# Performance work log

Hardware: AMD Instinct MI355X
Metric: run time of the kernel (lower is better)

Reference implementation:

```python
import jax, jax.numpy as jnp
import numpy as np

B, T, C = 4, 2048, 1024
N_HEAD = 16
HEAD_SIZE = C // N_HEAD


def setup_inputs() -> dict:
    key = jax.random.key(0)
    ks = jax.random.split(key, 9)
    std = 0.02
    return {
        "x": jax.random.normal(ks[0], (B, T, C), dtype=jnp.float32),
        "Wk": jax.random.normal(ks[1], (C, C), dtype=jnp.float32) * std,
        "bk": jnp.zeros((C,), dtype=jnp.float32),
        "Wq": jax.random.normal(ks[2], (C, C), dtype=jnp.float32) * std,
        "bq": jnp.zeros((C,), dtype=jnp.float32),
        "Wv": jax.random.normal(ks[3], (C, C), dtype=jnp.float32) * std,
        "bv": jnp.zeros((C,), dtype=jnp.float32),
        "Wo": jax.random.normal(ks[4], (C, C), dtype=jnp.float32) * std,
        "bo": jnp.zeros((C,), dtype=jnp.float32),
    }


def reference(x, Wk, bk, Wq, bq, Wv, bv, Wo, bo):
    # QKV projections -> (B, T, H, D)
    k = (x @ Wk + bk).reshape(B, T, N_HEAD, HEAD_SIZE)
    q = (x @ Wq + bq).reshape(B, T, N_HEAD, HEAD_SIZE)
    v = (x @ Wv + bv).reshape(B, T, N_HEAD, HEAD_SIZE)
    # Scaled causal attention scores: (B, H, T, T)
    scale = 1.0 / jnp.sqrt(jnp.asarray(HEAD_SIZE, dtype=x.dtype))
    scores = jnp.einsum("bqhd,bkhd->bhqk", q, k) * scale
    causal = jnp.tril(jnp.ones((T, T), dtype=bool))
    scores = jnp.where(causal, scores, jnp.asarray(-1e10, dtype=x.dtype))
    probs = jax.nn.softmax(scores, axis=-1)
    # Weighted values -> (B, T, H, D) -> (B, T, C)
    y = jnp.einsum("bhqk,bkhd->bqhd", probs, v).reshape(B, T, C)
    # Output projection (dropout rates are 0 / deterministic)
    return y @ Wo + bo
```

## Files before the change

kernel.cpp:

```cpp
#include <hip/hip_runtime.h>
#include <hip/hip_bf16.h>

typedef unsigned short ushort_t;
typedef __attribute__((ext_vector_type(8))) short short8;
typedef __attribute__((ext_vector_type(4))) float floatx4;

#define BATCH 4
#define SEQ   2048
#define CH    1024
#define NHEAD 16
#define HSZ   64
#define MROWS (BATCH * SEQ)

#define GLD16(gptr, lptr) \
    __builtin_amdgcn_global_load_lds((const __attribute__((address_space(1))) unsigned int*)(gptr), \
                                     (__attribute__((address_space(3))) unsigned int*)(lptr), 16, 0, 0)

__device__ inline ushort_t f2b(float f) {
    __hip_bfloat16 h = __float2bfloat16(f);
    return *(ushort_t*)&h;
}
__device__ inline float b2f(ushort_t u) {
    return __bfloat162float(*(__hip_bfloat16*)&u);
}

__device__ __forceinline__ float fast_exp2(float x) {
#if __has_builtin(__builtin_amdgcn_exp2f)
    return __builtin_amdgcn_exp2f(x);
#else
    float r; asm("v_exp_f32 %0, %1" : "=v"(r) : "v"(x)); return r;
#endif
}

__global__ void detect_dtype(const ushort_t* __restrict__ x, int* __restrict__ flag) {
    int cnt = 0;
    #pragma unroll
    for (int i = 0; i < 8; i++) {
        const int e = (x[2 * (threadIdx.x * 8 + i)] >> 7) & 0xFF;
        const unsigned long long m = __ballot(e >= 100 && e <= 140);
        cnt += (int)__popcll(m);
    }
    if (threadIdx.x == 0) *flag = (cnt >= 400) ? 1 : 0;
}

__global__ __launch_bounds__(256) void convert_wt4(const void* w0, const void* w1,
                                                   const void* w2, const void* w3,
                                                   ushort_t* o0, ushort_t* o1,
                                                   ushort_t* o2, ushort_t* o3,
                                                   const int* __restrict__ flag) {
    __shared__ ushort_t tile[32][33];
    const void* in = (blockIdx.z == 0) ? w0 : (blockIdx.z == 1) ? w1 : (blockIdx.z == 2) ? w2 : w3;
    ushort_t*  out = (blockIdx.z == 0) ? o0 : (blockIdx.z == 1) ? o1 : (blockIdx.z == 2) ? o2 : o3;
    const int am = *flag;
    const int bx = blockIdx.x * 32, by = blockIdx.y * 32;
    const int tx = threadIdx.x & 31, ty = threadIdx.x >> 5;
    #pragma unroll
    for (int r = ty; r < 32; r += 8) {
        const size_t idx = (size_t)(by + r) * CH + bx + tx;
        tile[r][tx] = am ? ((const ushort_t*)in)[idx] : f2b(((const float*)in)[idx]);
    }
    __syncthreads();
    #pragma unroll
    for (int r = ty; r < 32; r += 8)
        out[(size_t)(bx + r) * CH + by + tx] = tile[tx][r];
}

__global__ void convert_bias4(const void* b0, const void* b1, const void* b2, const void* b3,
                              ushort_t* __restrict__ out, const int* __restrict__ flag) {
    const int i = blockIdx.x * 256 + threadIdx.x;
    const int m = i >> 10, idx = i & 1023;
    const void* in = (m == 0) ? b0 : (m == 1) ? b1 : (m == 2) ? b2 : b3;
    out[i] = (*flag) ? ((const ushort_t*)in)[idx] : f2b(((const float*)in)[idx]);
}

__global__ __launch_bounds__(256) void convert_x(const void* __restrict__ in,
                                                 ushort_t* __restrict__ out,
                                                 const int* __restrict__ flag) {
    const int i = (blockIdx.x * 256 + threadIdx.x) * 8;
    if (*flag) {
        *(float4*)&out[i] = *(const float4*)&((const ushort_t*)in)[i];
    } else {
        const float* p = (const float*)in + i;
        float4 f0 = *(const float4*)p;
        float4 f1 = *(const float4*)(p + 4);
        ushort_t t[8] = {f2b(f0.x), f2b(f0.y), f2b(f0.z), f2b(f0.w),
                         f2b(f1.x), f2b(f1.y), f2b(f1.z), f2b(f1.w)};
        *(float4*)&out[i] = *(const float4*)t;
    }
}

__device__ __forceinline__ void kloop64(const ushort_t* __restrict__ A,
                                        const ushort_t* __restrict__ Bt,
                                        int K, int row0, int col0,
                                        ushort_t* As, ushort_t* Bs,
                                        floatx4 acc[4][4],
                                        int lane, int wave) {
    const int lane15 = lane & 15, quad = lane >> 4;
    const int wr = (wave >> 1) * 64, wc = (wave & 1) * 64;
    const int rg = lane >> 3;
    const int cg = (lane & 7) ^ rg;
    const int s7 = lane15 & 7;
    for (int k0 = 0; k0 < K; k0 += 64) {
        #pragma unroll
        for (int l = wave; l < 16; l += 4) {
            GLD16(A  + (size_t)(row0 + l * 8 + rg) * K + k0 + cg * 8, &As[l * 512]);
            GLD16(Bt + (size_t)(col0 + l * 8 + rg) * K + k0 + cg * 8, &Bs[l * 512]);
        }
        __syncthreads();
        #pragma unroll
        for (int kk = 0; kk < 2; kk++) {
            short8 af[4], bfr[4];
            #pragma unroll
            for (int i = 0; i < 4; i++)
                af[i] = *(const short8*)&As[(wr + i * 16 + lane15) * 64 + (((kk * 4 + quad) ^ s7) * 8)];
            #pragma unroll
            for (int j = 0; j < 4; j++)
                bfr[j] = *(const short8*)&Bs[(wc + j * 16 + lane15) * 64 + (((kk * 4 + quad) ^ s7) * 8)];
            #pragma unroll
            for (int i = 0; i < 4; i++)
                #pragma unroll
                for (int j = 0; j < 4; j++)
                    acc[i][j] = __builtin_amdgcn_mfma_f32_16x16x32_bf16(af[i], bfr[j], acc[i][j], 0, 0, 0);
        }
        __syncthreads();
    }
}

__global__ __launch_bounds__(256) void gemm_qkv(const ushort_t* __restrict__ A,
                                                const ushort_t* __restrict__ Bt,
                                                const ushort_t* __restrict__ bias,
                                                ushort_t* __restrict__ Qb,
                                                ushort_t* __restrict__ Kb,
                                                ushort_t* __restrict__ Vt,
                                                float qscale) {
    __shared__ __align__(16) ushort_t As[128 * 64];
    __shared__ __align__(16) ushort_t Bs[128 * 64];
    const int tid = threadIdx.x;
    const int lane = tid & 63, wave = tid >> 6;
    const int lane15 = lane & 15, quad = lane >> 4;
    const int wr = (wave >> 1) * 64, wc = (wave & 1) * 64;
    const int row0 = blockIdx.x * 128, col0 = blockIdx.y * 128;
    const int seg = blockIdx.y >> 3;

    floatx4 acc[4][4];
    #pragma unroll
    for (int i = 0; i < 4; i++)
        #pragma unroll
        for (int j = 0; j < 4; j++) acc[i][j] = {0.f, 0.f, 0.f, 0.f};

    kloop64(A, Bt, CH, row0, col0, As, Bs, acc, lane, wave);

    #pragma unroll
    for (int j = 0; j < 4; j++) {
        const int col = col0 + wc + j * 16 + lane15;
        const float bv = b2f(bias[col]);
        #pragma unroll
        for (int i = 0; i < 4; i++) {
            const int rowb = row0 + wr + i * 16 + quad * 4;
            if (seg == 0) {
                #pragma unroll
                for (int r = 0; r < 4; r++)
                    Qb[(size_t)(rowb + r) * CH + col] = f2b((acc[i][j][r] + bv) * qscale);
            } else if (seg == 1) {
                const int c = col - 1024;
                #pragma unroll
                for (int r = 0; r < 4; r++)
                    Kb[(size_t)(rowb + r) * CH + c] = f2b(acc[i][j][r] + bv);
            } else {
                const int c = col - 2048;
                ushort_t pk[4];
                #pragma unroll
                for (int r = 0; r < 4; r++) pk[r] = f2b(acc[i][j][r] + bv);
                const int bb = rowb >> 11, t = rowb & 2047;
                *(uint2*)&Vt[((size_t)bb * 1024 + c) * 2048 + t] = *(const uint2*)pk;
            }
        }
    }
}

__global__ __launch_bounds__(256) void gemm_bt(const ushort_t* __restrict__ A,
                                               const ushort_t* __restrict__ Bt,
                                               const ushort_t* __restrict__ bias,
                                               void* __restrict__ Out,
                                               int M, int N, int K,
                                               const int* __restrict__ oflag) {
    __shared__ __align__(16) ushort_t As[128 * 64];
    __shared__ __align__(16) ushort_t Bs[128 * 64];
    const int om = *oflag;
    const int tid = threadIdx.x;
    const int lane = tid & 63, wave = tid >> 6;
    const int lane15 = lane & 15, quad = lane >> 4;
    const int wr = (wave >> 1) * 64, wc = (wave & 1) * 64;
    const int row0 = blockIdx.x * 128, col0 = blockIdx.y * 128;

    floatx4 acc[4][4];
    #pragma unroll
    for (int i = 0; i < 4; i++)
        #pragma unroll
        for (int j = 0; j < 4; j++) acc[i][j] = {0.f, 0.f, 0.f, 0.f};

    kloop64(A, Bt, K, row0, col0, As, Bs, acc, lane, wave);

    #pragma unroll
    for (int j = 0; j < 4; j++) {
        const int col = col0 + wc + j * 16 + lane15;
        const float bv = b2f(bias[col]);
        #pragma unroll
        for (int i = 0; i < 4; i++) {
            const int rowb = row0 + wr + i * 16 + quad * 4;
            #pragma unroll
            for (int r = 0; r < 4; r++) {
                const float val = acc[i][j][r] + bv;
                const size_t idx = (size_t)(rowb + r) * N + col;
                if (om) ((ushort_t*)Out)[idx] = f2b(val);
                else    ((float*)Out)[idx] = val;
            }
        }
    }
}

__global__ __launch_bounds__(256) void attn_fwd(ushort_t* __restrict__ QY,
                                                const ushort_t* __restrict__ K,
                                                const ushort_t* __restrict__ Vt) {
    __shared__ __align__(16) ushort_t Ks[2][64 * 64];
    __shared__ __align__(16) ushort_t Vs[2][64 * 64];
    __shared__ __align__(16) ushort_t Ps[4 * 32 * 64];
    const int tid = threadIdx.x;
    const int lane = tid & 63, wave = tid >> 6;
    const int lane15 = lane & 15, quad = lane >> 4;
    const int sw = lane15 & 7;
    const int bid = blockIdx.x;
    const int hb = bid & 63, qslot = bid >> 6;
    const int qb = 15 - qslot;
    const int h = hb & 15, b = hb >> 4;
    const int q0 = qb * 128;
    const size_t baseR = (size_t)b * SEQ * CH + h * HSZ;
    const size_t baseV = ((size_t)b * 1024 + h * HSZ) * SEQ;
    const int rg = lane >> 3, cg = (lane & 7) ^ rg;
    const int psBase = wave * 2048;

    short8 qf[2][2];
    #pragma unroll
    for (int mm = 0; mm < 2; mm++) {
        const ushort_t* qp = QY + baseR + (size_t)(q0 + wave * 32 + mm * 16 + lane15) * CH + quad * 8;
        qf[mm][0] = *(const short8*)qp;
        qf[mm][1] = *(const short8*)(qp + 32);
    }
    const short8 kOnes = (short8)(short)0x3F80;

    floatx4 o[2][5];
    #pragma unroll
    for (int mm = 0; mm < 2; mm++)
        #pragma unroll
        for (int j = 0; j < 5; j++) o[mm][j] = {0.f, 0.f, 0.f, 0.f};

    const int nkt = 2 * qb + 2;
    #pragma unroll
    for (int l = wave; l < 8; l += 4) {
        GLD16(K  + baseR + (size_t)(l * 8 + rg) * CH + cg * 8, &Ks[0][l * 512]);
        GLD16(Vt + baseV + (size_t)(l * 8 + rg) * SEQ + cg * 8, &Vs[0][l * 512]);
    }

    for (int kt = 0; kt < nkt; kt++) {
        __syncthreads();
        const int cur = kt & 1;
        if (kt + 1 < nkt) {
            const int kv1 = (kt + 1) * 64, nb = cur ^ 1;
            #pragma unroll
            for (int l = wave; l < 8; l += 4) {
                GLD16(K  + baseR + (size_t)(kv1 + l * 8 + rg) * CH + cg * 8, &Ks[nb][l * 512]);
                GLD16(Vt + baseV + (size_t)(l * 8 + rg) * SEQ + kv1 + cg * 8, &Vs[nb][l * 512]);
            }
        }
        const int kv0 = kt * 64;
        const int masked = (kt >= 2 * qb);

        short8 kf[4][2];
        #pragma unroll
        for (int g = 0; g < 4; g++) {
            kf[g][0] = *(const short8*)&Ks[cur][(g * 16 + lane15) * 64 + ((quad ^ sw) * 8)];
            kf[g][1] = *(const short8*)&Ks[cur][(g * 16 + lane15) * 64 + (((quad + 4) ^ sw) * 8)];
        }

        #pragma unroll
        for (int mm = 0; mm < 2; mm++) {
            const int qrow = q0 + wave * 32 + mm * 16 + lane15;
            const int rowOff = psBase + (mm * 16 + lane15) * 64;
            #pragma unroll
            for (int g = 0; g < 4; g++) {
                floatx4 z = {0.f, 0.f, 0.f, 0.f};
                z = __builtin_amdgcn_mfma_f32_16x16x32_bf16(kf[g][0], qf[mm][0], z, 0, 0, 0);
                z = __builtin_amdgcn_mfma_f32_16x16x32_bf16(kf[g][1], qf[mm][1], z, 0, 0, 0);
                if (masked) {
                    #pragma unroll
                    for (int r = 0; r < 4; r++) {
                        const int col = kv0 + g * 16 + quad * 4 + r;
                        z[r] = (col <= qrow) ? z[r] : -1e30f;
                    }
                }
                const float p0 = fast_exp2(z[0]), p1 = fast_exp2(z[1]);
                const float p2 = fast_exp2(z[2]), p3 = fast_exp2(z[3]);
                unsigned int lo, hi;
                asm("v_cvt_pk_bf16_f32 %0, %1, %2" : "=v"(lo) : "v"(p0), "v"(p1));
                asm("v_cvt_pk_bf16_f32 %0, %1, %2" : "=v"(hi) : "v"(p2), "v"(p3));
                uint2 w; w.x = lo; w.y = hi;
                *(uint2*)&Ps[rowOff + (((g * 4 + quad) ^ lane15) * 4)] = w;
            }
        }

        #pragma unroll
        for (int kk = 0; kk < 2; kk++) {
            #pragma unroll
            for (int mm = 0; mm < 2; mm++) {
                const int rowOff = psBase + (mm * 16 + lane15) * 64;
                const int c0 = kk * 8 + quad * 2;
                short8 a;
                ((uint2*)&a)[0] = *(const uint2*)&Ps[rowOff + (((c0    ) ^ lane15) * 4)];
                ((uint2*)&a)[1] = *(const uint2*)&Ps[rowOff + (((c0 + 1) ^ lane15) * 4)];
                #pragma unroll
                for (int jn = 0; jn < 4; jn++) {
                    short8 bb = *(const short8*)&Vs[cur][(jn * 16 + lane15) * 64 + (((kk * 4 + quad) ^ sw) * 8)];
                    o[mm][jn] = __builtin_amdgcn_mfma_f32_16x16x32_bf16(a, bb, o[mm][jn], 0, 0, 0);
                }
                o[mm][4] = __builtin_amdgcn_mfma_f32_16x16x32_bf16(a, kOnes, o[mm][4], 0, 0, 0);
            }
        }
    }

    #pragma unroll
    for (int mm = 0; mm < 2; mm++)
        #pragma unroll
        for (int r = 0; r < 4; r++) {
            const int qrow = q0 + wave * 32 + mm * 16 + quad * 4 + r;
            const float rinv = 1.0f / fmaxf(o[mm][4][r], 1e-30f);
            #pragma unroll
            for (int jn = 0; jn < 4; jn++)
                QY[baseR + (size_t)qrow * CH + jn * 16 + lane15] = f2b(o[mm][jn][r] * rinv);
        }
}

extern "C" void kernel_launch(void* const* d_in, const int* in_sizes, int n_in,
                              void* d_out, int out_size, void* d_ws, size_t ws_size,
                              hipStream_t stream) {
    const void* x  = d_in[0];
    const void* Wk = d_in[1];
    const void* bk = d_in[2];
    const void* Wq = d_in[3];
    const void* bq = d_in[4];
    const void* Wv = d_in[5];
    const void* bv = d_in[6];
    const void* Wo = d_in[7];
    const void* bo = d_in[8];

    ushort_t* ws    = (ushort_t*)d_ws;
    int*      flag  = (int*)d_ws;
    ushort_t* biasC = ws + 2048;
    ushort_t* WqkvT = ws + 32768;
    ushort_t* WoT   = WqkvT + 3u * (1u << 20);
    ushort_t* xb    = ws + 4227072;
    ushort_t* Qb    = ws + 12615680;
    ushort_t* Kb    = (ushort_t*)d_out;
    ushort_t* VtB   = Kb + (size_t)MROWS * CH;

    detect_dtype<<<1, 64, 0, stream>>>((const ushort_t*)x, flag);

    dim3 tgrid(32, 32, 4);
    convert_wt4<<<tgrid, 256, 0, stream>>>(Wq, Wk, Wv, Wo,
                                           WqkvT, WqkvT + (1u << 20), WqkvT + 2u * (1u << 20), WoT, flag);
    convert_bias4<<<16, 256, 0, stream>>>(bq, bk, bv, bo, biasC, flag);
    convert_x<<<MROWS * CH / (256 * 8), 256, 0, stream>>>(x, xb, flag);

    dim3 qgrid(MROWS / 128, 3 * CH / 128);
    gemm_qkv<<<qgrid, 256, 0, stream>>>(xb, WqkvT, biasC, Qb, Kb, VtB, 0.1803368801f);

    attn_fwd<<<dim3(1024), 256, 0, stream>>>(Qb, Kb, VtB);

    dim3 ogrid(MROWS / 128, CH / 128);
    gemm_bt<<<ogrid, 256, 0, stream>>>(Qb, WoT, biasC + 3072, d_out, MROWS, CH, CH, flag);
}
```

Baseline: 247.9 us.

## Double-buffer LDS tiles in GEMM k-loop to overlap global loads with MFMA

```diff
diff --git a/kernel.cpp b/kernel.cpp
--- a/kernel.cpp
+++ b/kernel.cpp
@@ -89,6 +89,18 @@
     }
 }
 
+__device__ __forceinline__ void stage64(const ushort_t* __restrict__ A,
+                                        const ushort_t* __restrict__ Bt,
+                                        int K, int row0, int col0, int k0,
+                                        ushort_t* As, ushort_t* Bs,
+                                        int rg, int cg, int wave) {
+    #pragma unroll
+    for (int l = wave; l < 16; l += 4) {
+        GLD16(A  + (size_t)(row0 + l * 8 + rg) * K + k0 + cg * 8, &As[l * 512]);
+        GLD16(Bt + (size_t)(col0 + l * 8 + rg) * K + k0 + cg * 8, &Bs[l * 512]);
+    }
+}
+
 __device__ __forceinline__ void kloop64(const ushort_t* __restrict__ A,
                                         const ushort_t* __restrict__ Bt,
                                         int K, int row0, int col0,
@@ -100,29 +112,37 @@
     const int rg = lane >> 3;
     const int cg = (lane & 7) ^ rg;
     const int s7 = lane15 & 7;
+
+    stage64(A, Bt, K, row0, col0, 0, As, Bs, rg, cg, wave);
+    int cur = 0;
     for (int k0 = 0; k0 < K; k0 += 64) {
-        #pragma unroll
-        for (int l = wave; l < 16; l += 4) {
-            GLD16(A  + (size_t)(row0 + l * 8 + rg) * K + k0 + cg * 8, &As[l * 512]);
-            GLD16(Bt + (size_t)(col0 + l * 8 + rg) * K + k0 + cg * 8, &Bs[l * 512]);
-        }
-        __syncthreads();
+        if (k0 + 64 < K) {
+            const int nb = cur ^ 1;
+            stage64(A, Bt, K, row0, col0, k0 + 64, As + nb * 8192, Bs + nb * 8192, rg, cg, wave);
+            asm volatile("s_waitcnt vmcnt(8)" ::: "memory");
+        } else {
+            asm volatile("s_waitcnt vmcnt(0)" ::: "memory");
+        }
+        __builtin_amdgcn_s_barrier();
+        const ushort_t* Ac = As + cur * 8192;
+        const ushort_t* Bc = Bs + cur * 8192;
         #pragma unroll
         for (int kk = 0; kk < 2; kk++) {
             short8 af[4], bfr[4];
             #pragma unroll
             for (int i = 0; i < 4; i++)
-                af[i] = *(const short8*)&As[(wr + i * 16 + lane15) * 64 + (((kk * 4 + quad) ^ s7) * 8)];
+                af[i] = *(const short8*)&Ac[(wr + i * 16 + lane15) * 64 + (((kk * 4 + quad) ^ s7) * 8)];
             #pragma unroll
             for (int j = 0; j < 4; j++)
-                bfr[j] = *(const short8*)&Bs[(wc + j * 16 + lane15) * 64 + (((kk * 4 + quad) ^ s7) * 8)];
+                bfr[j] = *(const short8*)&Bc[(wc + j * 16 + lane15) * 64 + (((kk * 4 + quad) ^ s7) * 8)];
             #pragma unroll
             for (int i = 0; i < 4; i++)
                 #pragma unroll
                 for (int j = 0; j < 4; j++)
                     acc[i][j] = __builtin_amdgcn_mfma_f32_16x16x32_bf16(af[i], bfr[j], acc[i][j], 0, 0, 0);
         }
-        __syncthreads();
+        __builtin_amdgcn_s_barrier();
+        cur ^= 1;
     }
 }
 
@@ -133,8 +153,8 @@
                                                 ushort_t* __restrict__ Kb,
                                                 ushort_t* __restrict__ Vt,
                                                 float qscale) {
-    __shared__ __align__(16) ushort_t As[128 * 64];
-    __shared__ __align__(16) ushort_t Bs[128 * 64];
+    __shared__ __align__(16) ushort_t As[2 * 128 * 64];
+    __shared__ __align__(16) ushort_t Bs[2 * 128 * 64];
     const int tid = threadIdx.x;
     const int lane = tid & 63, wave = tid >> 6;
     const int lane15 = lane & 15, quad = lane >> 4;
@@ -184,8 +204,8 @@
                                                void* __restrict__ Out,
                                                int M, int N, int K,
                                                const int* __restrict__ oflag) {
-    __shared__ __align__(16) ushort_t As[128 * 64];
-    __shared__ __align__(16) ushort_t Bs[128 * 64];
+    __shared__ __align__(16) ushort_t As[2 * 128 * 64];
+    __shared__ __align__(16) ushort_t Bs[2 * 128 * 64];
     const int om = *oflag;
     const int tid = threadIdx.x;
     const int lane = tid & 63, wave = tid >> 6;
```

Result: no change. 246.3 us (-0.6%).

## Replace QKV GEMM with 256x256 double-buffered 8-wave pipelined kernel

Applied to the files above, without the earlier changes.

```diff
diff --git a/kernel.cpp b/kernel.cpp
--- a/kernel.cpp
+++ b/kernel.cpp
@@ -89,6 +89,117 @@
     }
 }
 
+#define STG(Sbuf, src, base0, h, tt) do {                                              \
+    const int r0_ = (h) * 128 + wave * 8 + lrow;                                       \
+    GLD16((src) + (size_t)((base0) + r0_) * CH + (tt) * 64 + gu * 8,                   \
+          &Sbuf[(tt) & 1][r0_ * 64 + lu * 8]);                                         \
+    GLD16((src) + (size_t)((base0) + r0_ + 64) * CH + (tt) * 64 + gu * 8,              \
+          &Sbuf[(tt) & 1][(r0_ + 64) * 64 + lu * 8]);                                  \
+} while (0)
+
+__global__ __launch_bounds__(512) void gemm_qkv8(const ushort_t* __restrict__ A,
+                                                 const ushort_t* __restrict__ Bt,
+                                                 const ushort_t* __restrict__ bias,
+                                                 ushort_t* __restrict__ Qb,
+                                                 ushort_t* __restrict__ Kb,
+                                                 ushort_t* __restrict__ Vt,
+                                                 float qscale) {
+    __shared__ __align__(16) ushort_t As[2][256 * 64];
+    __shared__ __align__(16) ushort_t Bs[2][256 * 64];
+    const int tid = threadIdx.x;
+    const int lane = tid & 63, wave = tid >> 6;
+    const int wm = wave >> 2, wn = wave & 3;
+    const int lane15 = lane & 15, quad = lane >> 4;
+    const int s7 = lane15 & 7;
+    const int lrow = lane >> 3, lu = lane & 7;
+    const int gu = lu ^ lrow;
+    const int cpx = (int)gridDim.x >> 3;
+    const int bidl = ((int)blockIdx.x & 7) * cpx + ((int)blockIdx.x >> 3);
+    const int rowblk = bidl / 12, colblk = bidl - rowblk * 12;
+    const int row0 = rowblk * 256, col0 = colblk * 256;
+    const int seg = col0 >> 10;
+
+    floatx4 acc[8][4];
+    #pragma unroll
+    for (int m = 0; m < 8; m++)
+        #pragma unroll
+        for (int n = 0; n < 4; n++) acc[m][n] = {0.f, 0.f, 0.f, 0.f};
+
+    STG(Bs, Bt, col0, 0, 0); STG(Bs, Bt, col0, 1, 0);
+    STG(As, A, row0, 0, 0);  STG(As, A, row0, 1, 0);
+
+    for (int t = 0; t < 16; ++t) {
+        const ushort_t* Ab = &As[t & 1][wm * 128 * 64];
+        const ushort_t* Bb = &Bs[t & 1][wn * 64 * 64];
+        const bool pf = (t + 1 < 16);
+        short8 bfr[4][2];
+        #pragma unroll
+        for (int p = 0; p < 4; ++p) {
+            if (p == 0) {
+                if (pf) { STG(Bs, Bt, col0, 0, t + 1); asm volatile("s_waitcnt vmcnt(2)" ::: "memory"); }
+                else    {                              asm volatile("s_waitcnt vmcnt(0)" ::: "memory"); }
+            } else if (pf) {
+                if (p == 1)      STG(Bs, Bt, col0, 1, t + 1);
+                else if (p == 2) STG(As, A, row0, 0, t + 1);
+                else             STG(As, A, row0, 1, t + 1);
+            }
+            __builtin_amdgcn_s_barrier();
+            if (p == 0) {
+                #pragma unroll
+                for (int n = 0; n < 4; ++n) {
+                    const int br = n * 16 + lane15;
+                    bfr[n][0] = *(const short8*)&Bb[br * 64 + ((quad ^ s7) * 8)];
+                    bfr[n][1] = *(const short8*)&Bb[br * 64 + (((quad + 4) ^ s7) * 8)];
+                }
+            }
+            short8 af[2][2];
+            #pragma unroll
+            for (int mi = 0; mi < 2; ++mi) {
+                const int ar = (p * 2 + mi) * 16 + lane15;
+                af[mi][0] = *(const short8*)&Ab[ar * 64 + ((quad ^ s7) * 8)];
+                af[mi][1] = *(const short8*)&Ab[ar * 64 + (((quad + 4) ^ s7) * 8)];
+            }
+            __builtin_amdgcn_s_setprio(1);
+            #pragma unroll
+            for (int mi = 0; mi < 2; ++mi)
+                #pragma unroll
+                for (int n = 0; n < 4; ++n) {
+                    acc[p * 2 + mi][n] = __builtin_amdgcn_mfma_f32_16x16x32_bf16(af[mi][0], bfr[n][0], acc[p * 2 + mi][n], 0, 0, 0);
+                    acc[p * 2 + mi][n] = __builtin_amdgcn_mfma_f32_16x16x32_bf16(af[mi][1], bfr[n][1], acc[p * 2 + mi][n], 0, 0, 0);
+                }
+            __builtin_amdgcn_s_setprio(0);
+            __builtin_amdgcn_s_barrier();
+        }
+    }
+
+    #pragma unroll
+    for (int n = 0; n < 4; ++n) {
+        const int col = col0 + wn * 64 + n * 16 + lane15;
+        const float bv = b2f(bias[col]);
+        #pragma unroll
+        for (int m = 0; m < 8; ++m) {
+            const int rowb = row0 + wm * 128 + m * 16 + quad * 4;
+            if (seg == 0) {
+                #pragma unroll
+                for (int r = 0; r < 4; r++)
+                    Qb[(size_t)(rowb + r) * CH + col] = f2b((acc[m][n][r] + bv) * qscale);
+            } else if (seg == 1) {
+                const int c = col - 1024;
+                #pragma unroll
+                for (int r = 0; r < 4; r++)
+                    Kb[(size_t)(rowb + r) * CH + c] = f2b(acc[m][n][r] + bv);
+            } else {
+                const int c = col - 2048;
+                ushort_t pk[4];
+                #pragma unroll
+                for (int r = 0; r < 4; r++) pk[r] = f2b(acc[m][n][r] + bv);
+                const int bb = rowb >> 11, tc = rowb & 2047;
+                *(uint2*)&Vt[((size_t)bb * 1024 + c) * 2048 + tc] = *(const uint2*)pk;
+            }
+        }
+    }
+}
+
 __device__ __forceinline__ void kloop64(const ushort_t* __restrict__ A,
                                         const ushort_t* __restrict__ Bt,
                                         int K, int row0, int col0,
@@ -123,58 +234,6 @@
                     acc[i][j] = __builtin_amdgcn_mfma_f32_16x16x32_bf16(af[i], bfr[j], acc[i][j], 0, 0, 0);
         }
         __syncthreads();
-    }
-}
-
-__global__ __launch_bounds__(256) void gemm_qkv(const ushort_t* __restrict__ A,
-                                                const ushort_t* __restrict__ Bt,
-                                                const ushort_t* __restrict__ bias,
-                                                ushort_t* __restrict__ Qb,
-                                                ushort_t* __restrict__ Kb,
-                                                ushort_t* __restrict__ Vt,
-                                                float qscale) {
-    __shared__ __align__(16) ushort_t As[128 * 64];
-    __shared__ __align__(16) ushort_t Bs[128 * 64];
-    const int tid = threadIdx.x;
-    const int lane = tid & 63, wave = tid >> 6;
-    const int lane15 = lane & 15, quad = lane >> 4;
-    const int wr = (wave >> 1) * 64, wc = (wave & 1) * 64;
-    const int row0 = blockIdx.x * 128, col0 = blockIdx.y * 128;
-    const int seg = blockIdx.y >> 3;
-
-    floatx4 acc[4][4];
-    #pragma unroll
-    for (int i = 0; i < 4; i++)
-        #pragma unroll
-        for (int j = 0; j < 4; j++) acc[i][j] = {0.f, 0.f, 0.f, 0.f};
-
-    kloop64(A, Bt, CH, row0, col0, As, Bs, acc, lane, wave);
-
-    #pragma unroll
-    for (int j = 0; j < 4; j++) {
-        const int col = col0 + wc + j * 16 + lane15;
-        const float bv = b2f(bias[col]);
-        #pragma unroll
-        for (int i = 0; i < 4; i++) {
-            const int rowb = row0 + wr + i * 16 + quad * 4;
-            if (seg == 0) {
-                #pragma unroll
-                for (int r = 0; r < 4; r++)
-                    Qb[(size_t)(rowb + r) * CH + col] = f2b((acc[i][j][r] + bv) * qscale);
-            } else if (seg == 1) {
-                const int c = col - 1024;
-                #pragma unroll
-                for (int r = 0; r < 4; r++)
-                    Kb[(size_t)(rowb + r) * CH + c] = f2b(acc[i][j][r] + bv);
-            } else {
-                const int c = col - 2048;
-                ushort_t pk[4];
-                #pragma unroll
-                for (int r = 0; r < 4; r++) pk[r] = f2b(acc[i][j][r] + bv);
-                const int bb = rowb >> 11, t = rowb & 2047;
-                *(uint2*)&Vt[((size_t)bb * 1024 + c) * 2048 + t] = *(const uint2*)pk;
-            }
-        }
     }
 }
 
@@ -370,8 +429,7 @@
     convert_bias4<<<16, 256, 0, stream>>>(bq, bk, bv, bo, biasC, flag);
     convert_x<<<MROWS * CH / (256 * 8), 256, 0, stream>>>(x, xb, flag);
 
-    dim3 qgrid(MROWS / 128, 3 * CH / 128);
-    gemm_qkv<<<qgrid, 256, 0, stream>>>(xb, WqkvT, biasC, Qb, Kb, VtB, 0.1803368801f);
+    gemm_qkv8<<<dim3(384), 512, 0, stream>>>(xb, WqkvT, biasC, Qb, Kb, VtB, 0.1803368801f);
 
     attn_fwd<<<dim3(1024), 256, 0, stream>>>(Qb, Kb, VtB);
 
```

Result: slower. 276.4 us (+11.5%).

## Use 256x128 triple-buffered 8-wave GEMM pipeline with XCD-aware block remap

Applied to the files above, without the earlier changes.

```diff
diff --git a/kernel.cpp b/kernel.cpp
--- a/kernel.cpp
+++ b/kernel.cpp
@@ -89,58 +89,86 @@
     }
 }
 
-__device__ __forceinline__ void kloop64(const ushort_t* __restrict__ A,
-                                        const ushort_t* __restrict__ Bt,
-                                        int K, int row0, int col0,
-                                        ushort_t* As, ushort_t* Bs,
-                                        floatx4 acc[4][4],
-                                        int lane, int wave) {
+__device__ __forceinline__ void pipe256x128(const ushort_t* __restrict__ A,
+                                            const ushort_t* __restrict__ Bt,
+                                            int row0, int col0,
+                                            ushort_t* __restrict__ As,
+                                            ushort_t* __restrict__ Bs,
+                                            floatx4 acc[4][4], int tid) {
+    const int lane = tid & 63, wave = tid >> 6;
     const int lane15 = lane & 15, quad = lane >> 4;
-    const int wr = (wave >> 1) * 64, wc = (wave & 1) * 64;
-    const int rg = lane >> 3;
-    const int cg = (lane & 7) ^ rg;
     const int s7 = lane15 & 7;
-    for (int k0 = 0; k0 < K; k0 += 64) {
-        #pragma unroll
-        for (int l = wave; l < 16; l += 4) {
-            GLD16(A  + (size_t)(row0 + l * 8 + rg) * K + k0 + cg * 8, &As[l * 512]);
-            GLD16(Bt + (size_t)(col0 + l * 8 + rg) * K + k0 + cg * 8, &Bs[l * 512]);
-        }
-        __syncthreads();
-        #pragma unroll
-        for (int kk = 0; kk < 2; kk++) {
+    const int wm = wave >> 1, wn = wave & 1;
+    const int lrow = lane >> 3, lu = lane & 7, gu = lu ^ lrow;
+    const int brow = tid >> 3, bu = tid & 7, bgu = bu ^ (brow & 7);
+
+    auto stage_part = [&](int buf, int tt, int h) {
+        ushort_t* Ad = As + buf * (256 * 64) + (h * 128 + wave * 16 + lrow) * 64 + lu * 8;
+        const ushort_t* Asrc = A + (size_t)(row0 + h * 128 + wave * 16 + lrow) * CH + tt * 64 + gu * 8;
+        GLD16(Asrc, Ad);
+        GLD16(Asrc + 8 * CH, Ad + 8 * 64);
+        ushort_t* Bd = Bs + buf * (128 * 64) + (h * 64 + brow) * 64 + bu * 8;
+        const ushort_t* Bsrc = Bt + (size_t)(col0 + h * 64 + brow) * CH + tt * 64 + bgu * 8;
+        GLD16(Bsrc, Bd);
+    };
+
+    stage_part(0, 0, 0); stage_part(0, 0, 1);
+    stage_part(1, 1, 0); stage_part(1, 1, 1);
+    asm volatile("s_waitcnt vmcnt(6)" ::: "memory");
+    __builtin_amdgcn_s_barrier();
+
+    int buf = 0;
+    for (int t = 0; t < 16; ++t) {
+        const ushort_t* Ab = As + buf * (256 * 64) + (wm * 64) * 64;
+        const ushort_t* Bb = Bs + buf * (128 * 64) + (wn * 64) * 64;
+        int bnext = buf + 2; if (bnext >= 3) bnext -= 3;
+        const bool pf = (t + 2 < 16);
+        #pragma unroll
+        for (int kk = 0; kk < 2; ++kk) {
             short8 af[4], bfr[4];
             #pragma unroll
             for (int i = 0; i < 4; i++)
-                af[i] = *(const short8*)&As[(wr + i * 16 + lane15) * 64 + (((kk * 4 + quad) ^ s7) * 8)];
+                af[i] = *(const short8*)&Ab[(i * 16 + lane15) * 64 + (((kk * 4 + quad) ^ s7) * 8)];
             #pragma unroll
             for (int j = 0; j < 4; j++)
-                bfr[j] = *(const short8*)&Bs[(wc + j * 16 + lane15) * 64 + (((kk * 4 + quad) ^ s7) * 8)];
+                bfr[j] = *(const short8*)&Bb[(j * 16 + lane15) * 64 + (((kk * 4 + quad) ^ s7) * 8)];
+            if (pf) stage_part(bnext, t + 2, kk);
+            __builtin_amdgcn_s_barrier();
+            __builtin_amdgcn_s_setprio(1);
             #pragma unroll
             for (int i = 0; i < 4; i++)
                 #pragma unroll
                 for (int j = 0; j < 4; j++)
                     acc[i][j] = __builtin_amdgcn_mfma_f32_16x16x32_bf16(af[i], bfr[j], acc[i][j], 0, 0, 0);
-        }
-        __syncthreads();
-    }
-}
-
-__global__ __launch_bounds__(256) void gemm_qkv(const ushort_t* __restrict__ A,
-                                                const ushort_t* __restrict__ Bt,
-                                                const ushort_t* __restrict__ bias,
-                                                ushort_t* __restrict__ Qb,
-                                                ushort_t* __restrict__ Kb,
-                                                ushort_t* __restrict__ Vt,
-                                                float qscale) {
-    __shared__ __align__(16) ushort_t As[128 * 64];
-    __shared__ __align__(16) ushort_t Bs[128 * 64];
+            __builtin_amdgcn_s_setprio(0);
+            if (kk == 1 && t < 15) {
+                if (pf) asm volatile("s_waitcnt vmcnt(6)" ::: "memory");
+                else    asm volatile("s_waitcnt vmcnt(0)" ::: "memory");
+            }
+            __builtin_amdgcn_s_barrier();
+        }
+        buf = (buf == 2) ? 0 : buf + 1;
+    }
+}
+
+__global__ __launch_bounds__(512) void gemm_qkv8(const ushort_t* __restrict__ A,
+                                                 const ushort_t* __restrict__ Bt,
+                                                 const ushort_t* __restrict__ bias,
+                                                 ushort_t* __restrict__ Qb,
+                                                 ushort_t* __restrict__ Kb,
+                                                 ushort_t* __restrict__ Vt,
+                                                 float qscale) {
+    __shared__ __align__(16) ushort_t As[3 * 256 * 64];
+    __shared__ __align__(16) ushort_t Bs[3 * 128 * 64];
     const int tid = threadIdx.x;
     const int lane = tid & 63, wave = tid >> 6;
     const int lane15 = lane & 15, quad = lane >> 4;
-    const int wr = (wave >> 1) * 64, wc = (wave & 1) * 64;
-    const int row0 = blockIdx.x * 128, col0 = blockIdx.y * 128;
-    const int seg = blockIdx.y >> 3;
+    const int wm = wave >> 1, wn = wave & 1;
+    const int bid = blockIdx.x;
+    const int bidl = (bid & 7) * 96 + (bid >> 3);
+    const int rowblk = bidl / 24, colblk = bidl - rowblk * 24;
+    const int row0 = rowblk * 256, col0 = colblk * 128;
+    const int seg = col0 >> 10;
 
     floatx4 acc[4][4];
     #pragma unroll
@@ -148,15 +176,15 @@
         #pragma unroll
         for (int j = 0; j < 4; j++) acc[i][j] = {0.f, 0.f, 0.f, 0.f};
 
-    kloop64(A, Bt, CH, row0, col0, As, Bs, acc, lane, wave);
+    pipe256x128(A, Bt, row0, col0, As, Bs, acc, tid);
 
     #pragma unroll
     for (int j = 0; j < 4; j++) {
-        const int col = col0 + wc + j * 16 + lane15;
+        const int col = col0 + wn * 64 + j * 16 + lane15;
         const float bv = b2f(bias[col]);
         #pragma unroll
         for (int i = 0; i < 4; i++) {
-            const int rowb = row0 + wr + i * 16 + quad * 4;
+            const int rowb = row0 + wm * 64 + i * 16 + quad * 4;
             if (seg == 0) {
                 #pragma unroll
                 for (int r = 0; r < 4; r++)
@@ -171,27 +199,29 @@
                 ushort_t pk[4];
                 #pragma unroll
                 for (int r = 0; r < 4; r++) pk[r] = f2b(acc[i][j][r] + bv);
-                const int bb = rowb >> 11, t = rowb & 2047;
-                *(uint2*)&Vt[((size_t)bb * 1024 + c) * 2048 + t] = *(const uint2*)pk;
-            }
-        }
-    }
-}
-
-__global__ __launch_bounds__(256) void gemm_bt(const ushort_t* __restrict__ A,
-                                               const ushort_t* __restrict__ Bt,
-                                               const ushort_t* __restrict__ bias,
-                                               void* __restrict__ Out,
-                                               int M, int N, int K,
-                                               const int* __restrict__ oflag) {
-    __shared__ __align__(16) ushort_t As[128 * 64];
-    __shared__ __align__(16) ushort_t Bs[128 * 64];
+                const int bb = rowb >> 11, tc = rowb & 2047;
+                *(uint2*)&Vt[((size_t)bb * 1024 + c) * 2048 + tc] = *(const uint2*)pk;
+            }
+        }
+    }
+}
+
+__global__ __launch_bounds__(512) void gemm_bt8(const ushort_t* __restrict__ A,
+                                                const ushort_t* __restrict__ Bt,
+                                                const ushort_t* __restrict__ bias,
+                                                void* __restrict__ Out,
+                                                const int* __restrict__ oflag) {
+    __shared__ __align__(16) ushort_t As[3 * 256 * 64];
+    __shared__ __align__(16) ushort_t Bs[3 * 128 * 64];
     const int om = *oflag;
     const int tid = threadIdx.x;
     const int lane = tid & 63, wave = tid >> 6;
     const int lane15 = lane & 15, quad = lane >> 4;
-    const int wr = (wave >> 1) * 64, wc = (wave & 1) * 64;
-    const int row0 = blockIdx.x * 128, col0 = blockIdx.y * 128;
+    const int wm = wave >> 1, wn = wave & 1;
+    const int bid = blockIdx.x;
+    const int bidl = (bid & 7) * 32 + (bid >> 3);
+    const int rowblk = bidl >> 3, colblk = bidl & 7;
+    const int row0 = rowblk * 256, col0 = colblk * 128;
 
     floatx4 acc[4][4];
     #pragma unroll
@@ -199,19 +229,19 @@
         #pragma unroll
         for (int j = 0; j < 4; j++) acc[i][j] = {0.f, 0.f, 0.f, 0.f};
 
-    kloop64(A, Bt, K, row0, col0, As, Bs, acc, lane, wave);
+    pipe256x128(A, Bt, row0, col0, As, Bs, acc, tid);
 
     #pragma unroll
     for (int j = 0; j < 4; j++) {
-        const int col = col0 + wc + j * 16 + lane15;
+        const int col = col0 + wn * 64 + j * 16 + lane15;
         const float bv = b2f(bias[col]);
         #pragma unroll
         for (int i = 0; i < 4; i++) {
-            const int rowb = row0 + wr + i * 16 + quad * 4;
+            const int rowb = row0 + wm * 64 + i * 16 + quad * 4;
             #pragma unroll
             for (int r = 0; r < 4; r++) {
                 const float val = acc[i][j][r] + bv;
-                const size_t idx = (size_t)(rowb + r) * N + col;
+                const size_t idx = (size_t)(rowb + r) * CH + col;
                 if (om) ((ushort_t*)Out)[idx] = f2b(val);
                 else    ((float*)Out)[idx] = val;
             }
@@ -370,11 +400,9 @@
     convert_bias4<<<16, 256, 0, stream>>>(bq, bk, bv, bo, biasC, flag);
     convert_x<<<MROWS * CH / (256 * 8), 256, 0, stream>>>(x, xb, flag);
 
-    dim3 qgrid(MROWS / 128, 3 * CH / 128);
-    gemm_qkv<<<qgrid, 256, 0, stream>>>(xb, WqkvT, biasC, Qb, Kb, VtB, 0.1803368801f);
+    gemm_qkv8<<<dim3(768), 512, 0, stream>>>(xb, WqkvT, biasC, Qb, Kb, VtB, 0.1803368801f);
 
     attn_fwd<<<dim3(1024), 256, 0, stream>>>(Qb, Kb, VtB);
 
-    dim3 ogrid(MROWS / 128, CH / 128);
-    gemm_bt<<<ogrid, 256, 0, stream>>>(Qb, WoT, biasC + 3072, d_out, MROWS, CH, CH, flag);
-}
+    gemm_bt8<<<dim3(256), 512, 0, stream>>>(Qb, WoT, biasC + 3072, d_out, flag);
+}
```

Result: no change. 243.8 us (-1.6%).
